# Kernel tuning notes

Measured on AMD Instinct MI355X. Metric: run time of the kernel, lower is better.

## Reference

```python
import jax, jax.numpy as jnp
import numpy as np

EMBED_DIM = 1024
N_HEADS = 16
HEAD_DIM = EMBED_DIM // N_HEADS


def setup_inputs() -> dict:
    key = jax.random.key(0)
    k_x, k_wqkv, k_bqkv, k_wo, k_bo = jax.random.split(key, 5)
    s = 1.0 / np.sqrt(EMBED_DIM)
    return {
        "x": jax.random.normal(k_x, (2, 2048, EMBED_DIM), dtype=jnp.float32),
        "w_qkv": jax.random.uniform(k_wqkv, (EMBED_DIM, 3 * EMBED_DIM), jnp.float32, -s, s),
        "b_qkv": jax.random.uniform(k_bqkv, (3 * EMBED_DIM,), jnp.float32, -s, s),
        "w_out": jax.random.uniform(k_wo, (EMBED_DIM, EMBED_DIM), jnp.float32, -s, s),
        "b_out": jax.random.uniform(k_bo, (EMBED_DIM,), jnp.float32, -s, s),
    }


def reference(x, w_qkv, b_qkv, w_out, b_out):
    B, T, C = x.shape
    qkv = x @ w_qkv + b_qkv                      # [B,T,3C]
    q, k, v = jnp.split(qkv, 3, axis=-1)
    # [B,T,C] -> [B,H,T,D]
    def heads(t):
        return t.reshape(B, T, N_HEADS, HEAD_DIM).transpose(0, 2, 1, 3)
    q, k, v = heads(q), heads(k), heads(v)
    scale = 1.0 / np.sqrt(HEAD_DIM).astype(np.float32)
    scores = jnp.einsum("bhqd,bhkd->bhqk", q, k) * scale
    causal = jnp.tril(jnp.ones((T, T), dtype=bool))  # True where allowed
    scores = jnp.where(causal, scores, jnp.finfo(scores.dtype).min)
    attn = jax.nn.softmax(scores, axis=-1)
    out = jnp.einsum("bhqk,bhkd->bhqd", attn, v)
    out = out.transpose(0, 2, 1, 3).reshape(B, T, C)
    return out @ w_out + b_out
```

## Files before the change

kernel.cpp:

```cpp
#include <hip/hip_runtime.h>
#include <hip/hip_bf16.h>

typedef __attribute__((ext_vector_type(4))) float f32x4;
typedef __attribute__((ext_vector_type(8))) short bf16x8;

static __device__ __forceinline__ unsigned short f2bf(float f) {
  union { float f; unsigned u; } v;
  v.f = f;
  unsigned r = v.u + 0x7FFFu + ((v.u >> 16) & 1u);
  return (unsigned short)(r >> 16);
}

static __device__ __forceinline__ unsigned cvt_pk_bf16(float lo, float hi) {
  unsigned r;
  asm("v_cvt_pk_bf16_f32 %0, %1, %2" : "=v"(r) : "v"(lo), "v"(hi));
  return r;
}

static __device__ __forceinline__ void gload16(const void* g, void* lds) {
  __builtin_amdgcn_global_load_lds(
      (const __attribute__((address_space(1))) unsigned int*)g,
      (__attribute__((address_space(3))) unsigned int*)lds, 16, 0, 0);
}

__global__ __launch_bounds__(256) void prep_kernel(
    const float* __restrict__ x, const float* __restrict__ w_qkv,
    const float* __restrict__ w_out, unsigned short* __restrict__ xb,
    unsigned short* __restrict__ wqkvT, unsigned short* __restrict__ woT) {
  __shared__ float tile[32][33];
  const int bid = blockIdx.x, tid = threadIdx.x;
  if (bid < 4096) {
    int i = bid * 256 + tid;
    float4 v = reinterpret_cast<const float4*>(x)[i];
    ushort4 o;
    o.x = f2bf(v.x); o.y = f2bf(v.y); o.z = f2bf(v.z); o.w = f2bf(v.w);
    reinterpret_cast<ushort4*>(xb)[i] = o;
    return;
  }
  const float* src; unsigned short* dst; int c0, r0, C;
  if (bid < 7168) {
    int t = bid - 4096;
    src = w_qkv; dst = wqkvT; C = 3072;
    c0 = (t % 96) * 32; r0 = (t / 96) * 32;
  } else {
    int t = bid - 7168;
    src = w_out; dst = woT; C = 1024;
    c0 = (t & 31) * 32; r0 = (t >> 5) * 32;
  }
  int tx = tid & 31, ty = tid >> 5;
#pragma unroll
  for (int i = 0; i < 32; i += 8)
    tile[ty + i][tx] = src[(size_t)(r0 + ty + i) * C + c0 + tx];
  __syncthreads();
#pragma unroll
  for (int i = 0; i < 32; i += 8)
    dst[(size_t)(c0 + ty + i) * 1024 + r0 + tx] = f2bf(tile[tx][ty + i]);
}

template <int MODE, int BN>
__global__ __launch_bounds__(256, MODE == 0 ? 3 : 2) void gemm_bf16(
    const unsigned short* __restrict__ A,
    const unsigned short* __restrict__ Bt,
    const float* __restrict__ bias,
    unsigned short* __restrict__ q_out,
    unsigned short* __restrict__ k_out,
    unsigned short* __restrict__ v_out,
    float* __restrict__ f_out) {
  constexpr int NB2 = BN / 32;
  constexpr int NBL = BN / 64;
  __shared__ __align__(16) unsigned short As[2][128 * 32];
  __shared__ __align__(16) unsigned short Bs[2][BN * 32];

  const int tid = threadIdx.x;
  const int wid = tid >> 6, lane = tid & 63;
  const int l15 = lane & 15, g = lane >> 4;
  const int wm = wid >> 1, wn = wid & 1;
  const int n0 = blockIdx.x * BN, m0 = blockIdx.y * 128;

  f32x4 acc[4][NB2] = {};

  auto stage = [&](int k0, int bsel) {
#pragma unroll
    for (int i = 0; i < 2; ++i) {
      int t = tid + i * 256;
      int row = t >> 2, c8 = (t & 3) << 3;
      gload16(A + (size_t)(m0 + row) * 1024 + k0 + c8, &As[bsel][(i * 256 + wid * 64) * 8]);
    }
#pragma unroll
    for (int i = 0; i < NBL; ++i) {
      int t = tid + i * 256;
      int row = t >> 2, c8 = (t & 3) << 3;
      gload16(Bt + (size_t)(n0 + row) * 1024 + k0 + c8, &Bs[bsel][(i * 256 + wid * 64) * 8]);
    }
  };

  stage(0, 0);
  __syncthreads();
  for (int ks = 0; ks < 32; ++ks) {
    const int cur = ks & 1;
    if (ks + 1 < 32) stage((ks + 1) * 32, cur ^ 1);
    bf16x8 a[4], b[NB2];
#pragma unroll
    for (int mi = 0; mi < 4; ++mi)
      a[mi] = *reinterpret_cast<const bf16x8*>(&As[cur][(wm * 64 + mi * 16 + l15) * 32 + g * 8]);
#pragma unroll
    for (int ni = 0; ni < NB2; ++ni)
      b[ni] = *reinterpret_cast<const bf16x8*>(&Bs[cur][(wn * (BN / 2) + ni * 16 + l15) * 32 + g * 8]);
    __builtin_amdgcn_s_setprio(1);
#pragma unroll
    for (int mi = 0; mi < 4; ++mi)
#pragma unroll
      for (int ni = 0; ni < NB2; ++ni)
        acc[mi][ni] = __builtin_amdgcn_mfma_f32_16x16x32_bf16(a[mi], b[ni], acc[mi][ni], 0, 0, 0);
    __builtin_amdgcn_s_setprio(0);
    __syncthreads();
  }

  if (MODE == 0) {
    const int which = n0 >> 10;
    unsigned short* dst = (which == 0) ? q_out : (which == 1) ? k_out : v_out;
    const float oscale = (which == 0) ? 0.125f * 1.44269504f : 1.0f;
#pragma unroll
    for (int ni = 0; ni < NB2; ++ni) {
      int col = n0 + wn * (BN / 2) + ni * 16 + l15;
      int c = col & 1023;
      int h = c >> 6, d = c & 63;
      float bv = bias[col];
#pragma unroll
      for (int mi = 0; mi < 4; ++mi) {
#pragma unroll
        for (int r = 0; r < 4; ++r) {
          int rowg = m0 + wm * 64 + mi * 16 + g * 4 + r;
          int bb = rowg >> 11, tt = rowg & 2047;
          dst[((bb * 16 + h) * 2048 + tt) * 64 + d] = f2bf((acc[mi][ni][r] + bv) * oscale);
        }
      }
    }
  } else {
#pragma unroll
    for (int ni = 0; ni < NB2; ++ni) {
      int col = n0 + wn * (BN / 2) + ni * 16 + l15;
      float bv = bias[col];
#pragma unroll
      for (int mi = 0; mi < 4; ++mi)
#pragma unroll
        for (int r = 0; r < 4; ++r) {
          int rowg = m0 + wm * 64 + mi * 16 + g * 4 + r;
          f_out[(size_t)rowg * 1024 + col] = acc[mi][ni][r] + bv;
        }
    }
  }
}

#define KS_SZ (64 * 64)
#define VT_SZ (64 * 64)

__device__ __forceinline__ void attn_stage_K(const unsigned short* __restrict__ Kb,
                                             int k0, unsigned short* KsBuf,
                                             int tid, int wid) {
#pragma unroll
  for (int i = 0; i < 2; ++i) {
    int t = tid + i * 256;
    int row = t >> 3;
    int cb = (t & 7) << 4;
    int src = cb ^ ((row & 7) << 4);
    gload16((const char*)Kb + (size_t)(k0 + row) * 128 + src,
            (char*)KsBuf + (i * 256 + wid * 64) * 16);
  }
}

__device__ __forceinline__ void write_vt(unsigned short* VtBuf, int kvL, int d8,
                                         uint4 v0, uint4 v1) {
  char* base = (char*)VtBuf + (size_t)d8 * 128;
  const int c = kvL * 2;
  unsigned lo, hi;
  lo = __builtin_amdgcn_perm(v1.x, v0.x, 0x05040100u);
  hi = __builtin_amdgcn_perm(v1.x, v0.x, 0x07060302u);
  *reinterpret_cast<unsigned*>(base + 0 * 128 + (c ^ (0 << 4))) = lo;
  *reinterpret_cast<unsigned*>(base + 1 * 128 + (c ^ (1 << 4))) = hi;
  lo = __builtin_amdgcn_perm(v1.y, v0.y, 0x05040100u);
  hi = __builtin_amdgcn_perm(v1.y, v0.y, 0x07060302u);
  *reinterpret_cast<unsigned*>(base + 2 * 128 + (c ^ (2 << 4))) = lo;
  *reinterpret_cast<unsigned*>(base + 3 * 128 + (c ^ (3 << 4))) = hi;
  lo = __builtin_amdgcn_perm(v1.z, v0.z, 0x05040100u);
  hi = __builtin_amdgcn_perm(v1.z, v0.z, 0x07060302u);
  *reinterpret_cast<unsigned*>(base + 4 * 128 + (c ^ (4 << 4))) = lo;
  *reinterpret_cast<unsigned*>(base + 5 * 128 + (c ^ (5 << 4))) = hi;
  lo = __builtin_amdgcn_perm(v1.w, v0.w, 0x05040100u);
  hi = __builtin_amdgcn_perm(v1.w, v0.w, 0x07060302u);
  *reinterpret_cast<unsigned*>(base + 6 * 128 + (c ^ (6 << 4))) = lo;
  *reinterpret_cast<unsigned*>(base + 7 * 128 + (c ^ (7 << 4))) = hi;
}

__global__ __launch_bounds__(256, 4) void attn_fwd(
    const unsigned short* __restrict__ Q,
    const unsigned short* __restrict__ K,
    const unsigned short* __restrict__ V,
    unsigned short* __restrict__ O) {
  __shared__ __align__(16) unsigned short Ks[2 * KS_SZ];
  __shared__ __align__(16) unsigned short Vt[2 * VT_SZ];
  __shared__ __align__(16) unsigned short Ps[64 * 64];

  const int tid = threadIdx.x;
  const int wid = tid >> 6;
  const int l15 = tid & 15;
  const int g = (tid & 63) >> 4;

  const int lin = blockIdx.x;
  const int bh = lin & 31;
  const int o = lin >> 5, oq = o & 7, os = o >> 3;
  const int qt = (os == 0) ? 31 - oq : (os == 1) ? 16 + oq : (os == 2) ? 15 - oq : oq;
  const int b = bh >> 4, h = bh & 15;
  const int q0 = qt << 6, nt = qt + 1;

  const unsigned short* Qb = Q + (size_t)bh * 2048 * 64;
  const unsigned short* Kb = K + (size_t)bh * 2048 * 64;
  const unsigned short* Vb = V + (size_t)bh * 2048 * 64;

  bf16x8 qf[2];
  {
    const unsigned short* qrow_p = Qb + (size_t)(q0 + wid * 16 + l15) * 64;
    qf[0] = *reinterpret_cast<const bf16x8*>(qrow_p + g * 8);
    qf[1] = *reinterpret_cast<const bf16x8*>(qrow_p + 32 + g * 8);
  }

  float m_run = -1e30f;
  float l_run = 0.0f;
  f32x4 ot[4] = {};
  const int qg = q0 + wid * 16 + l15;
  const int kvL = (tid & 31) * 2, d8 = (tid >> 5) * 8;
  const int qrow = wid * 16 + l15;
  const int sP = (qrow & 7) << 4;

  attn_stage_K(Kb, 0, Ks, tid, wid);
  {
    const uint4* vp = reinterpret_cast<const uint4*>(Vb + (size_t)kvL * 64 + d8);
    write_vt(Vt, kvL, d8, vp[0], vp[8]);
  }
  __syncthreads();

  for (int t = 0; t < nt; ++t) {
    const unsigned short* KsC = Ks + (t & 1) * KS_SZ;
    const unsigned short* VtC = Vt + (t & 1) * VT_SZ;
    uint4 va, vb;
    const bool pf = (t + 1 < nt);
    if (pf) {
      attn_stage_K(Kb, (t + 1) << 6, Ks + ((t + 1) & 1) * KS_SZ, tid, wid);
      const uint4* vp = reinterpret_cast<const uint4*>(
          Vb + (size_t)(((t + 1) << 6) + kvL) * 64 + d8);
      va = vp[0];
      vb = vp[8];
    }

    f32x4 s[4] = {};
    __builtin_amdgcn_s_setprio(1);
#pragma unroll
    for (int kk = 0; kk < 2; ++kk)
#pragma unroll
      for (int mi = 0; mi < 4; ++mi) {
        int row = mi * 16 + l15;
        int cb = (kk * 64 + g * 16) ^ ((row & 7) << 4);
        bf16x8 kf = *reinterpret_cast<const bf16x8*>((const char*)KsC + row * 128 + cb);
        s[mi] = __builtin_amdgcn_mfma_f32_16x16x32_bf16(kf, qf[kk], s[mi], 0, 0, 0);
      }
    __builtin_amdgcn_s_setprio(0);

    if (t == nt - 1) {
      const int k0 = t << 6;
#pragma unroll
      for (int mi = 0; mi < 4; ++mi)
#pragma unroll
        for (int r = 0; r < 4; ++r) {
          int kvg = k0 + mi * 16 + g * 4 + r;
          s[mi][r] = (kvg <= qg) ? s[mi][r] : -1e30f;
        }
    }

    float pmax = -1e30f;
#pragma unroll
    for (int mi = 0; mi < 4; ++mi)
#pragma unroll
      for (int r = 0; r < 4; ++r) pmax = fmaxf(pmax, s[mi][r]);

    if (!__all(pmax <= m_run + 8.0f)) {
      float tmax = fmaxf(pmax, __shfl_xor(pmax, 16));
      tmax = fmaxf(tmax, __shfl_xor(tmax, 32));
      float m_new = fmaxf(m_run, tmax);
      float corr = __builtin_amdgcn_exp2f(m_run - m_new);
      l_run *= corr;
#pragma unroll
      for (int mi = 0; mi < 4; ++mi)
#pragma unroll
        for (int r = 0; r < 4; ++r) ot[mi][r] *= corr;
      m_run = m_new;
    }

    float tsum = 0.f;
#pragma unroll
    for (int mi = 0; mi < 4; ++mi) {
      float p0 = __builtin_amdgcn_exp2f(s[mi][0] - m_run);
      float p1 = __builtin_amdgcn_exp2f(s[mi][1] - m_run);
      float p2 = __builtin_amdgcn_exp2f(s[mi][2] - m_run);
      float p3 = __builtin_amdgcn_exp2f(s[mi][3] - m_run);
      tsum += (p0 + p1) + (p2 + p3);
      uint2 pk;
      pk.x = cvt_pk_bf16(p0, p1);
      pk.y = cvt_pk_bf16(p2, p3);
      *reinterpret_cast<uint2*>((char*)Ps + qrow * 128 + ((mi * 32 + g * 8) ^ sP)) = pk;
    }
    l_run += tsum;

    __builtin_amdgcn_s_setprio(1);
#pragma unroll
    for (int kk = 0; kk < 2; ++kk) {
      bf16x8 pfr = *reinterpret_cast<const bf16x8*>(
          (const char*)Ps + qrow * 128 + ((kk * 64 + g * 16) ^ sP));
#pragma unroll
      for (int mi = 0; mi < 4; ++mi) {
        int row = mi * 16 + l15;
        bf16x8 vf = *reinterpret_cast<const bf16x8*>(
            (const char*)VtC + row * 128 + ((kk * 64 + g * 16) ^ ((row & 7) << 4)));
        ot[mi] = __builtin_amdgcn_mfma_f32_16x16x32_bf16(vf, pfr, ot[mi], 0, 0, 0);
      }
    }
    __builtin_amdgcn_s_setprio(0);

    if (pf) write_vt(Vt + ((t + 1) & 1) * VT_SZ, kvL, d8, va, vb);
    __syncthreads();
  }

  float l_tot = l_run + __shfl_xor(l_run, 16);
  l_tot += __shfl_xor(l_tot, 32);
  float inv_l = 1.0f / l_tot;

#pragma unroll
  for (int mi = 0; mi < 4; ++mi) {
    uint2 pk;
    pk.x = cvt_pk_bf16(ot[mi][0] * inv_l, ot[mi][1] * inv_l);
    pk.y = cvt_pk_bf16(ot[mi][2] * inv_l, ot[mi][3] * inv_l);
    int b0 = (mi * 32 + g * 8) ^ sP;
    *reinterpret_cast<uint2*>((char*)Ks + qrow * 128 + b0) = pk;
  }
  __syncthreads();
#pragma unroll
  for (int i = 0; i < 2; ++i) {
    int t = tid + i * 256;
    int row = t >> 3;
    int cb = (t & 7) << 4;
    int sw = cb ^ ((row & 7) << 4);
    bf16x8 vv = *reinterpret_cast<const bf16x8*>((const char*)Ks + row * 128 + sw);
    *reinterpret_cast<bf16x8*>(O + ((size_t)(b * 2048 + q0 + row)) * 1024 + h * 64 + (cb >> 1)) = vv;
  }
}

extern "C" void kernel_launch(void* const* d_in, const int* in_sizes, int n_in,
                              void* d_out, int out_size, void* d_ws, size_t ws_size,
                              hipStream_t stream) {
  const float* x = (const float*)d_in[0];
  const float* w_qkv = (const float*)d_in[1];
  const float* b_qkv = (const float*)d_in[2];
  const float* w_out = (const float*)d_in[3];
  const float* b_out = (const float*)d_in[4];
  float* out = (float*)d_out;
  char* ws = (char*)d_ws;

  unsigned short* xb    = (unsigned short*)d_out;
  unsigned short* wqkvT = (unsigned short*)(ws);
  unsigned short* woT   = (unsigned short*)(ws + 6291456);
  unsigned short* q_buf = (unsigned short*)(ws + 8388608);
  unsigned short* k_buf = (unsigned short*)(ws + 16777216);
  unsigned short* v_buf = (unsigned short*)(ws + 25165824);
  unsigned short* aout  = (unsigned short*)(ws + 33554432);

  prep_kernel<<<dim3(8192), dim3(256), 0, stream>>>(x, w_qkv, w_out, xb, wqkvT, woT);

  gemm_bf16<0, 128><<<dim3(24, 32), dim3(256), 0, stream>>>(
      xb, wqkvT, b_qkv, q_buf, k_buf, v_buf, nullptr);

  attn_fwd<<<dim3(1024), dim3(256), 0, stream>>>(q_buf, k_buf, v_buf, aout);

  gemm_bf16<1, 64><<<dim3(16, 32), dim3(256), 0, stream>>>(
      aout, woT, b_out, nullptr, nullptr, nullptr, out);
}
```

Measured before the change: 107.2 us.

## Replace QKV GEMM with 256x256-tile 8-phase pipelined kernel using swizzled LDS

The QKV projection GEMM moves from 128x128 tiles with 256 threads to 256x256 tiles with 512 threads (8 waves). The K loop is split into 8 phases, each interleaving half-tile global-to-LDS loads with MFMA work, with explicit vmcnt waits and barriers. LDS uses an XOR swizzle, and blocks are remapped across the 192-block grid for L2 locality. This targets more operand reuse per block and better overlap of loads with compute, at the cost of heavy register and LDS use (128 KB) and only 192 blocks, which may leave CUs idle.

```diff
diff --git a/kernel.cpp b/kernel.cpp
--- a/kernel.cpp
+++ b/kernel.cpp
@@ -57,17 +57,141 @@
     dst[(size_t)(c0 + ty + i) * 1024 + r0 + tx] = f2bf(tile[tx][ty + i]);
 }
 
-template <int MODE, int BN>
-__global__ __launch_bounds__(256, MODE == 0 ? 3 : 2) void gemm_bf16(
+__global__ __launch_bounds__(512, 2) void gemm_qkv_8ph(
     const unsigned short* __restrict__ A,
     const unsigned short* __restrict__ Bt,
     const float* __restrict__ bias,
     unsigned short* __restrict__ q_out,
     unsigned short* __restrict__ k_out,
-    unsigned short* __restrict__ v_out,
+    unsigned short* __restrict__ v_out) {
+  __shared__ __align__(16) char AsB[2 * 32768];
+  __shared__ __align__(16) char BsB[2 * 32768];
+
+  const int tid = threadIdx.x;
+  const int lane = tid & 63, wid = tid >> 6;
+  const int l15 = lane & 15, g = lane >> 4;
+  const int wm = wid >> 2, wn = wid & 3;
+
+  const int wg = blockIdx.x;
+  const int lin = (wg & 7) * 24 + (wg >> 3);
+  const int bx = lin >> 4, by = lin & 15;
+  const int n0 = bx * 256, m0 = by * 256;
+
+  const int srow = tid >> 3;
+  const int scb = (tid & 7) << 4;
+  const int sswz = scb ^ ((srow & 7) << 4);
+
+  auto stageHalf = [&](const unsigned short* mat, int rowbase, int kt, char* region) {
+#pragma unroll
+    for (int i = 0; i < 2; ++i) {
+      gload16((const char*)mat + ((size_t)(rowbase + srow + i * 64) * 1024 + kt * 64) * 2 + sswz,
+              region + (wid * 64 + i * 512) * 16);
+    }
+  };
+  auto rdA = [&](const char* Ab, int mi, int ks) -> bf16x8 {
+    int r = mi * 16 + l15;
+    int c = (ks * 64 + g * 16) ^ ((r & 7) << 4);
+    return *reinterpret_cast<const bf16x8*>(Ab + wm * 16384 + r * 128 + c);
+  };
+  auto rdB = [&](const char* Bb, int ni, int ks) -> bf16x8 {
+    int rr = wn * 64 + ni * 16 + l15;
+    int c = (ks * 64 + g * 16) ^ ((rr & 7) << 4);
+    return *reinterpret_cast<const bf16x8*>(Bb + (rr >> 7) * 16384 + (rr & 127) * 128 + c);
+  };
+
+  f32x4 acc[8][4] = {};
+
+  stageHalf(A, m0, 0, AsB);
+  stageHalf(A, m0 + 128, 0, AsB + 16384);
+  stageHalf(Bt, n0, 0, BsB);
+  stageHalf(Bt, n0 + 128, 0, BsB + 16384);
+  stageHalf(Bt, n0, 1, BsB + 32768);
+  stageHalf(Bt, n0 + 128, 1, BsB + 32768 + 16384);
+  asm volatile("s_waitcnt vmcnt(4)" ::: "memory");
+  __builtin_amdgcn_s_barrier();
+  __builtin_amdgcn_sched_barrier(0);
+
+  for (int it = 0; it < 8; ++it) {
+    const int kt0 = it * 2;
+    bf16x8 bfr[4][2];
+#pragma unroll
+    for (int ph = 0; ph < 8; ++ph) {
+      const int buf = ph >> 2, qd = ph & 3;
+      const char* Ab = AsB + buf * 32768;
+      const char* Bb = BsB + buf * 32768;
+      if (qd == 0) {
+#pragma unroll
+        for (int ni = 0; ni < 4; ++ni)
+#pragma unroll
+          for (int ks = 0; ks < 2; ++ks) bfr[ni][ks] = rdB(Bb, ni, ks);
+      }
+      bf16x8 af[2][2];
+#pragma unroll
+      for (int msub = 0; msub < 2; ++msub)
+#pragma unroll
+        for (int ks = 0; ks < 2; ++ks) af[msub][ks] = rdA(Ab, qd * 2 + msub, ks);
+
+      if (ph == 0) stageHalf(A, m0, kt0 + 1, AsB + 32768);
+      else if (ph == 1) stageHalf(A, m0 + 128, kt0 + 1, AsB + 32768 + 16384);
+      else if (it < 7) {
+        if (ph == 2) stageHalf(Bt, n0, kt0 + 2, BsB);
+        else if (ph == 3) stageHalf(Bt, n0 + 128, kt0 + 2, BsB + 16384);
+        else if (ph == 4) stageHalf(A, m0, kt0 + 2, AsB);
+        else if (ph == 5) stageHalf(A, m0 + 128, kt0 + 2, AsB + 16384);
+        else if (ph == 6) stageHalf(Bt, n0, kt0 + 3, BsB + 32768);
+        else stageHalf(Bt, n0 + 128, kt0 + 3, BsB + 32768 + 16384);
+      }
+      if (ph == 3) {
+        if (it == 7) { asm volatile("s_waitcnt vmcnt(0)" ::: "memory"); }
+        else         { asm volatile("s_waitcnt vmcnt(4)" ::: "memory"); }
+      } else if (ph == 7 && it < 7) {
+        asm volatile("s_waitcnt vmcnt(4)" ::: "memory");
+      }
+      __builtin_amdgcn_s_barrier();
+      __builtin_amdgcn_sched_barrier(0);
+
+      __builtin_amdgcn_s_setprio(1);
+#pragma unroll
+      for (int ks = 0; ks < 2; ++ks)
+#pragma unroll
+        for (int msub = 0; msub < 2; ++msub)
+#pragma unroll
+          for (int ni = 0; ni < 4; ++ni)
+            acc[qd * 2 + msub][ni] = __builtin_amdgcn_mfma_f32_16x16x32_bf16(
+                af[msub][ks], bfr[ni][ks], acc[qd * 2 + msub][ni], 0, 0, 0);
+      __builtin_amdgcn_s_setprio(0);
+      __builtin_amdgcn_s_barrier();
+      __builtin_amdgcn_sched_barrier(0);
+    }
+  }
+
+  const int which = n0 >> 10;
+  unsigned short* dst = (which == 0) ? q_out : (which == 1) ? k_out : v_out;
+  const float oscale = (which == 0) ? 0.125f * 1.44269504f : 1.0f;
+#pragma unroll
+  for (int ni = 0; ni < 4; ++ni) {
+    int col = n0 + wn * 64 + ni * 16 + l15;
+    int c = col & 1023;
+    int h = c >> 6, d = c & 63;
+    float bv = bias[col];
+#pragma unroll
+    for (int mi = 0; mi < 8; ++mi) {
+#pragma unroll
+      for (int r = 0; r < 4; ++r) {
+        int rowg = m0 + wm * 128 + mi * 16 + g * 4 + r;
+        int bb = rowg >> 11, tt = rowg & 2047;
+        dst[((bb * 16 + h) * 2048 + tt) * 64 + d] = f2bf((acc[mi][ni][r] + bv) * oscale);
+      }
+    }
+  }
+}
+
+__global__ __launch_bounds__(256, 2) void gemm_out(
+    const unsigned short* __restrict__ A,
+    const unsigned short* __restrict__ Bt,
+    const float* __restrict__ bias,
     float* __restrict__ f_out) {
-  constexpr int NB2 = BN / 32;
-  constexpr int NBL = BN / 64;
+  constexpr int BN = 64, NB2 = 2, NBL = 1;
   __shared__ __align__(16) unsigned short As[2][128 * 32];
   __shared__ __align__(16) unsigned short Bs[2][BN * 32];
 
@@ -116,39 +240,17 @@
     __syncthreads();
   }
 
-  if (MODE == 0) {
-    const int which = n0 >> 10;
-    unsigned short* dst = (which == 0) ? q_out : (which == 1) ? k_out : v_out;
-    const float oscale = (which == 0) ? 0.125f * 1.44269504f : 1.0f;
-#pragma unroll
-    for (int ni = 0; ni < NB2; ++ni) {
-      int col = n0 + wn * (BN / 2) + ni * 16 + l15;
-      int c = col & 1023;
-      int h = c >> 6, d = c & 63;
-      float bv = bias[col];
-#pragma unroll
-      for (int mi = 0; mi < 4; ++mi) {
-#pragma unroll
-        for (int r = 0; r < 4; ++r) {
-          int rowg = m0 + wm * 64 + mi * 16 + g * 4 + r;
-          int bb = rowg >> 11, tt = rowg & 2047;
-          dst[((bb * 16 + h) * 2048 + tt) * 64 + d] = f2bf((acc[mi][ni][r] + bv) * oscale);
-        }
-      }
-    }
-  } else {
-#pragma unroll
-    for (int ni = 0; ni < NB2; ++ni) {
-      int col = n0 + wn * (BN / 2) + ni * 16 + l15;
-      float bv = bias[col];
-#pragma unroll
-      for (int mi = 0; mi < 4; ++mi)
-#pragma unroll
-        for (int r = 0; r < 4; ++r) {
-          int rowg = m0 + wm * 64 + mi * 16 + g * 4 + r;
-          f_out[(size_t)rowg * 1024 + col] = acc[mi][ni][r] + bv;
-        }
-    }
+#pragma unroll
+  for (int ni = 0; ni < NB2; ++ni) {
+    int col = n0 + wn * (BN / 2) + ni * 16 + l15;
+    float bv = bias[col];
+#pragma unroll
+    for (int mi = 0; mi < 4; ++mi)
+#pragma unroll
+      for (int r = 0; r < 4; ++r) {
+        int rowg = m0 + wm * 64 + mi * 16 + g * 4 + r;
+        f_out[(size_t)rowg * 1024 + col] = acc[mi][ni][r] + bv;
+      }
   }
 }
 
@@ -374,11 +476,10 @@
 
   prep_kernel<<<dim3(8192), dim3(256), 0, stream>>>(x, w_qkv, w_out, xb, wqkvT, woT);
 
-  gemm_bf16<0, 128><<<dim3(24, 32), dim3(256), 0, stream>>>(
-      xb, wqkvT, b_qkv, q_buf, k_buf, v_buf, nullptr);
+  gemm_qkv_8ph<<<dim3(192), dim3(512), 0, stream>>>(
+      xb, wqkvT, b_qkv, q_buf, k_buf, v_buf);
 
   attn_fwd<<<dim3(1024), dim3(256), 0, stream>>>(q_buf, k_buf, v_buf, aout);
 
-  gemm_bf16<1, 64><<<dim3(16, 32), dim3(256), 0, stream>>>(
-      aout, woT, b_out, nullptr, nullptr, nullptr, out);
-}
+  gemm_out<<<dim3(16, 32), dim3(256), 0, stream>>>(aout, woT, b_out, out);
+}
```

Measured after the change: 108.7 us. Within noise of the previous version (+1.4%).
